# Kernel tuning notes

Hardware: AMD Instinct MI355X
Metric: run time of the kernel (lower is better)

Reference implementation:

```python
import jax, jax.numpy as jnp
import numpy as np

OUT, IN = 4096, 4096
GROUP = 128
N_GROUPS = IN // GROUP  # 32, remainder_cols == 0
BITS_PRIMARY = 4
BITS_RESIDUAL = 2
EPS = 1e-12


def setup_inputs() -> dict:
    key = jax.random.key(0)
    ks = jax.random.split(key, 6)
    return {
        "x": jax.random.normal(ks[0], (4, 2048, IN), dtype=jnp.float32),
        "norms_primary": jax.random.uniform(ks[1], (OUT, N_GROUPS), dtype=jnp.float32),
        "norms_residual": jax.random.uniform(ks[2], (OUT, N_GROUPS), dtype=jnp.float32),
        "bias": jax.random.normal(ks[3], (OUT,), dtype=jnp.float32),
        "idx_primary": jax.random.randint(ks[4], (OUT, N_GROUPS, GROUP), 0, 2 ** BITS_PRIMARY, dtype=jnp.int32),
        "idx_residual": jax.random.randint(ks[5], (OUT, N_GROUPS, GROUP), 0, 2 ** BITS_RESIDUAL, dtype=jnp.int32),
    }


def _dequant(idx, norms, bits):
    # Codebook: symmetric uniform levels in [-1, 1]; TurboQuant stores a
    # unit-direction per group (codes) plus its L2 norm (fp32 scale).
    levels = jnp.linspace(-1.0, 1.0, 2 ** bits, dtype=norms.dtype)
    q = levels[idx]                                             # [O, G, gs]
    unit = q * jax.lax.rsqrt(jnp.sum(q * q, axis=-1, keepdims=True) + EPS)
    w = norms[..., None] * unit                                 # [O, G, gs]
    return w.reshape(w.shape[0], -1)                            # [O, IN]


def reference(x, norms_primary, norms_residual, bias, idx_primary, idx_residual):
    # primary reconstruction + residual correction, then dense matmul
    w = _dequant(idx_primary, norms_primary, BITS_PRIMARY) \
        + _dequant(idx_residual, norms_residual, BITS_RESIDUAL)  # [OUT, IN]
    w = w.astype(x.dtype)
    # F.linear: y = x @ W^T + b
    return jnp.einsum('bsi,oi->bso', x, w) + bias.astype(x.dtype)
```

## Files before the change

### kernel.cpp

```cpp
#include <hip/hip_runtime.h>
#include <hip/hip_bf16.h>
#include <stdint.h>

#define OUT_DIM 4096
#define IN_DIM  4096
#define GROUPSZ 128
#define NGROUPS 32
#define M_TOTAL 8192
#define EPS_Q   1e-12f

#define BM 256
#define BN 256
#define BK 64
#define NT (IN_DIM / BK)

typedef float f32x4   __attribute__((ext_vector_type(4)));
typedef float float4v __attribute__((ext_vector_type(4)));
typedef short bf16x8  __attribute__((ext_vector_type(8)));

static __device__ __forceinline__ short f2bf(float f) {
    union { float f; unsigned u; } v; v.f = f;
    unsigned r = v.u + 0x7fffu + ((v.u >> 16) & 1u);
    return (short)(r >> 16);
}

#define GLOAD16(gp, lp) __builtin_amdgcn_global_load_lds( \
    (const __attribute__((address_space(1))) void*)(gp),  \
    (__attribute__((address_space(3))) void*)(lp), 16, 0, 0)

__global__ __launch_bounds__(256) void dequant_kernel(
    const float* __restrict__ norms_p, const float* __restrict__ norms_r,
    const int* __restrict__ idx_p, const int* __restrict__ idx_r,
    short* __restrict__ W)
{
    const int gid  = (int)((blockIdx.x * 256u + threadIdx.x) >> 6);
    const int lane = threadIdx.x & 63;
    const size_t base = (size_t)gid * GROUPSZ;

    const int ip0 = idx_p[base + lane];
    const int ip1 = idx_p[base + lane + 64];
    const int ir0 = idx_r[base + lane];
    const int ir1 = idx_r[base + lane + 64];

    const float qp0 = -1.f + (2.f / 15.f) * (float)ip0;
    const float qp1 = -1.f + (2.f / 15.f) * (float)ip1;
    const float qr0 = -1.f + (2.f / 3.f)  * (float)ir0;
    const float qr1 = -1.f + (2.f / 3.f)  * (float)ir1;

    float ssp = qp0 * qp0 + qp1 * qp1;
    float ssr = qr0 * qr0 + qr1 * qr1;
    #pragma unroll
    for (int m = 32; m >= 1; m >>= 1) {
        ssp += __shfl_xor(ssp, m);
        ssr += __shfl_xor(ssr, m);
    }
    const float sp = norms_p[gid] / sqrtf(ssp + EPS_Q);
    const float sr = norms_r[gid] / sqrtf(ssr + EPS_Q);

    W[base + lane]      = f2bf(qp0 * sp + qr0 * sr);
    W[base + lane + 64] = f2bf(qp1 * sp + qr1 * sr);
}

__global__ __launch_bounds__(256) void cast_kernel(
    const float* __restrict__ x, short* __restrict__ xb)
{
    const size_t i = ((size_t)blockIdx.x * 256u + threadIdx.x) * 8u;
    float4v a = *(const float4v*)(x + i);
    float4v b = *(const float4v*)(x + i + 4);
    bf16x8 o;
    o[0] = f2bf(a[0]); o[1] = f2bf(a[1]); o[2] = f2bf(a[2]); o[3] = f2bf(a[3]);
    o[4] = f2bf(b[0]); o[5] = f2bf(b[1]); o[6] = f2bf(b[2]); o[7] = f2bf(b[3]);
    *(bf16x8*)(xb + i) = o;
}

template<int HA, int HB>
__device__ __forceinline__ void mfma_quad(f32x4 (&acc)[2][2][4][2],
                                          const bf16x8 (&af)[4][2],
                                          const bf16x8 (&bf)[2][2]) {
#pragma unroll
    for (int m = 0; m < 4; ++m)
#pragma unroll
        for (int n = 0; n < 2; ++n)
#pragma unroll
            for (int kh = 0; kh < 2; ++kh)
                acc[HA][HB][m][n] = __builtin_amdgcn_mfma_f32_16x16x32_bf16(
                    af[m][kh], bf[n][kh], acc[HA][HB][m][n], 0, 0, 0);
}

static __device__ __forceinline__ void rd8(const short* base, int ck0, int ck1,
                                           bf16x8 (&f)[4][2]) {
#pragma unroll
    for (int m = 0; m < 4; ++m) {
        f[m][0] = *(const bf16x8*)(base + m * 1024 + ck0);
        f[m][1] = *(const bf16x8*)(base + m * 1024 + ck1);
    }
}

static __device__ __forceinline__ void rd4(const short* base, int ck0, int ck1,
                                           bf16x8 (&f)[2][2]) {
#pragma unroll
    for (int n = 0; n < 2; ++n) {
        f[n][0] = *(const bf16x8*)(base + n * 1024 + ck0);
        f[n][1] = *(const bf16x8*)(base + n * 1024 + ck1);
    }
}

#define BARRIER()  asm volatile("s_barrier" ::: "memory")
#define SCHEDBAR() __builtin_amdgcn_sched_barrier(0)
#define LGKMC(N)   do { asm volatile("s_waitcnt lgkmcnt(" #N ")" ::: "memory"); \
                        SCHEDBAR(); } while (0)
#define WAITV(N)   asm volatile("s_waitcnt vmcnt(" #N ")" ::: "memory")

__global__ __launch_bounds__(512, 2) void gemm_kernel(
    const short* __restrict__ Ag,
    const short* __restrict__ Bg,
    const float* __restrict__ bias,
    float* __restrict__ C)
{
    __shared__ short lds[65536];

    const int tid  = threadIdx.x;
    const int lane = tid & 63;
    const int wid  = tid >> 6;
    const int wr   = wid >> 2;
    const int wc   = wid & 3;
    const int fr   = lane & 15;
    const int lq   = lane >> 4;

    const int nwg = gridDim.x;
    const int cpx = nwg >> 3;
    const int wg  = ((int)blockIdx.x & 7) * cpx + ((int)blockIdx.x >> 3);
    const int ntile = wg & 15;
    const int mtile = wg >> 4;
    const uint32_t brow = (uint32_t)mtile * BM;
    const uint32_t bcol = (uint32_t)ntile * BN;

    const uint32_t sr_ = (uint32_t)(tid >> 3);
    const uint32_t gc_ = (uint32_t)((tid & 7) ^ ((tid >> 3) & 7));
    const uint32_t aOffB = (brow + sr_) * IN_DIM + gc_ * 8;
    const uint32_t bOffB = (bcol + sr_) * IN_DIM + gc_ * 8;

    auto stage = [&](const short* M, uint32_t baseOff, uint32_t extra, short* dstRegion) {
        GLOAD16(M + baseOff + extra,            dstRegion + tid * 8);
        GLOAD16(M + baseOff + extra + 262144u,  dstRegion + tid * 8 + 4096);
    };

    const int c0  = (lq ^ (fr & 7));
    const int ck0 = c0 * 8;
    const int ck1 = (c0 ^ 4) * 8;
    const int aRd = (wr * 64 + fr) * 64;
    const int bRd = (wc * 32 + fr) * 64;

    f32x4  acc[2][2][4][2] = {};
    bf16x8 af[4][2], af2[4][2], bf0[2][2], bf1[2][2];

    stage(Ag, aOffB, 0u,            lds);
    stage(Bg, bOffB, 0u,            lds + 16384);
    stage(Ag, aOffB, 524288u,       lds + 8192);
    stage(Bg, bOffB, 524288u,       lds + 24576);
    stage(Ag, aOffB, 64u,           lds + 32768);
    stage(Bg, bOffB, 64u,           lds + 32768 + 16384);
    WAITV(8);
    BARRIER();

#define TILE_BODY(T, STG0, STG1, STG2, STG3, WAIT_MID, WAIT_END, BAR_END) do { \
    short* sb = lds + (((T) & 1) ? 32768 : 0);                                \
    short* ob = lds + (((T) & 1) ? 0 : 32768);                                \
                              \
    rd8(sb + aRd, ck0, ck1, af);                                              \
    rd4(sb + 16384 + bRd, ck0, ck1, bf0);                                     \
    if (STG0) stage(Ag, aOffB, 524288u + (uint32_t)((T) + 1) * 64u, ob + 8192); \
    LGKMC(0);                                                                 \
    __builtin_amdgcn_s_setprio(1); mfma_quad<0,0>(acc, af, bf0);              \
    __builtin_amdgcn_s_setprio(0);                                            \
    WAIT_MID;                                                                 \
    BARRIER();                                                                \
                             \
    rd4(sb + 24576 + bRd, ck0, ck1, bf1);                                     \
    SCHEDBAR();                                                               \
    rd8(sb + 8192 + aRd, ck0, ck1, af2);                                      \
    if (STG1) stage(Bg, bOffB, 524288u + (uint32_t)((T) + 1) * 64u, ob + 24576); \
    LGKMC(8);                     \
    __builtin_amdgcn_s_setprio(1); mfma_quad<0,1>(acc, af, bf1);              \
    __builtin_amdgcn_s_setprio(0);                                            \
    if (STG2) stage(Ag, aOffB, (uint32_t)((T) + 2) * 64u, sb);                \
    LGKMC(0);                    \
    __builtin_amdgcn_s_setprio(1); mfma_quad<1,0>(acc, af2, bf0);             \
    __builtin_amdgcn_s_setprio(0);                                            \
    if (STG3) stage(Bg, bOffB, (uint32_t)((T) + 2) * 64u, sb + 16384);        \
    __builtin_amdgcn_s_setprio(1); mfma_quad<1,1>(acc, af2, bf1);             \
    __builtin_amdgcn_s_setprio(0);                                            \
    WAIT_END;                                                                 \
    if (BAR_END) BARRIER();                                                   \
} while (0)

    #pragma unroll 1
    for (int t = 0; t < NT - 2; ++t) {
        TILE_BODY(t, 1, 1, 1, 1, WAITV(6), WAITV(8), 1);
    }
    TILE_BODY(NT - 2, 1, 1, 0, 0, WAITV(6), WAITV(4), 1);
    TILE_BODY(NT - 1, 0, 0, 0, 0, WAITV(0), (void)0, 0);

    #pragma unroll
    for (int hA = 0; hA < 2; ++hA)
    #pragma unroll
    for (int hB = 0; hB < 2; ++hB)
    #pragma unroll
    for (int n = 0; n < 2; ++n) {
        const int col = (int)bcol + hB * 128 + wc * 32 + n * 16 + fr;
        const float bv = bias[col];
        #pragma unroll
        for (int m = 0; m < 4; ++m) {
            const size_t row0 = (size_t)brow + hA * 128 + wr * 64 + m * 16 + lq * 4;
            #pragma unroll
            for (int r = 0; r < 4; ++r)
                C[(row0 + r) * OUT_DIM + col] = acc[hA][hB][m][n][r] + bv;
        }
    }
#undef TILE_BODY
}

extern "C" void kernel_launch(void* const* d_in, const int* in_sizes, int n_in,
                              void* d_out, int out_size, void* d_ws, size_t ws_size,
                              hipStream_t stream)
{
    const float* x        = (const float*)d_in[0];
    const float* norms_p  = (const float*)d_in[1];
    const float* norms_r  = (const float*)d_in[2];
    const float* bias     = (const float*)d_in[3];
    const int*   idx_p    = (const int*)d_in[4];
    const int*   idx_r    = (const int*)d_in[5];
    float*       out      = (float*)d_out;

    short* xb = (short*)d_ws;
    short* wq = (short*)d_ws + (size_t)M_TOTAL * IN_DIM;

    dequant_kernel<<<(OUT_DIM * NGROUPS) / 4, 256, 0, stream>>>(
        norms_p, norms_r, idx_p, idx_r, wq);

    cast_kernel<<<(int)(((size_t)M_TOTAL * IN_DIM) / (256 * 8)), 256, 0, stream>>>(x, xb);

    gemm_kernel<<<(M_TOTAL / BM) * (OUT_DIM / BN), 512, 0, stream>>>(xb, wq, bias, out);
}
```

Measured before the change: 281.2 us.

## Restructure GEMM main loop into barrier-synchronized phases with reordered quadrant staging

Rewrites the bf16 MFMA GEMM main loop as a two-tile unrolled group body. LDS reads, global-to-LDS stage issues and the four MFMA quadrants now sit in separate phases divided by workgroup barriers, and the quadrant order and per-quadrant staging order change. The prologue now prefetches one more quarter-tile so the steady state can keep more loads in flight. The aim is more regular overlap of loads with compute across waves, at the cost of many more barriers per tile, which could serialize waves.

```diff
diff --git a/kernel.cpp b/kernel.cpp
--- a/kernel.cpp
+++ b/kernel.cpp
@@ -154,52 +154,61 @@
     f32x4  acc[2][2][4][2] = {};
     bf16x8 af[4][2], af2[4][2], bf0[2][2], bf1[2][2];
 
-    stage(Ag, aOffB, 0u,            lds);
-    stage(Bg, bOffB, 0u,            lds + 16384);
-    stage(Ag, aOffB, 524288u,       lds + 8192);
-    stage(Bg, bOffB, 524288u,       lds + 24576);
-    stage(Ag, aOffB, 64u,           lds + 32768);
-    stage(Bg, bOffB, 64u,           lds + 32768 + 16384);
-    WAITV(8);
+    stage(Ag, aOffB, 0u,             lds);
+    stage(Bg, bOffB, 0u,             lds + 16384);
+    stage(Bg, bOffB, 524288u,        lds + 24576);
+    stage(Ag, aOffB, 524288u,        lds + 8192);
+    stage(Ag, aOffB, 64u,            lds + 32768);
+    stage(Bg, bOffB, 64u,            lds + 32768 + 16384);
+    stage(Bg, bOffB, 524288u + 64u,  lds + 32768 + 24576);
+    WAITV(6);
     BARRIER();
 
-#define TILE_BODY(T, STG0, STG1, STG2, STG3, WAIT_MID, WAIT_END, BAR_END) do { \
-    short* sb = lds + (((T) & 1) ? 32768 : 0);                                \
-    short* ob = lds + (((T) & 1) ? 0 : 32768);                                \
-                              \
-    rd8(sb + aRd, ck0, ck1, af);                                              \
-    rd4(sb + 16384 + bRd, ck0, ck1, bf0);                                     \
-    if (STG0) stage(Ag, aOffB, 524288u + (uint32_t)((T) + 1) * 64u, ob + 8192); \
+#define GROUP_BODY(SB, OB, TT, S_A1, S_A0, S_B0, S_B1, WAIT_END) do {         \
+                  \
+    rd8((SB) + aRd, ck0, ck1, af);                                            \
+    rd4((SB) + 16384 + bRd, ck0, ck1, bf0);                                   \
+    if (S_A1) stage(Ag, aOffB, 524288u + (uint32_t)((TT)+1)*64u, (OB)+8192);  \
+    LGKMC(8);                                                                 \
+    BARRIER();                                                                \
     LGKMC(0);                                                                 \
     __builtin_amdgcn_s_setprio(1); mfma_quad<0,0>(acc, af, bf0);              \
     __builtin_amdgcn_s_setprio(0);                                            \
-    WAIT_MID;                                                                 \
-    BARRIER();                                                                \
-                             \
-    rd4(sb + 24576 + bRd, ck0, ck1, bf1);                                     \
+    BARRIER();                                                                \
+                         \
+    rd4((SB) + 24576 + bRd, ck0, ck1, bf1);                                   \
+    if (S_A0) stage(Ag, aOffB, (uint32_t)((TT)+2)*64u, (SB));                 \
+    BARRIER();                                                                \
+    LGKMC(0);                                                                 \
+    __builtin_amdgcn_s_setprio(1); mfma_quad<0,1>(acc, af, bf1);              \
+    __builtin_amdgcn_s_setprio(0);                                            \
+    BARRIER();                                                                \
+                         \
+    rd8((SB) + 8192 + aRd, ck0, ck1, af2);                                    \
+    if (S_B0) stage(Bg, bOffB, (uint32_t)((TT)+2)*64u, (SB)+16384);           \
+    BARRIER();                                                                \
+    LGKMC(0);                                                                 \
+    __builtin_amdgcn_s_setprio(1); mfma_quad<1,1>(acc, af2, bf1);             \
+    __builtin_amdgcn_s_setprio(0);                                            \
+    BARRIER();                                                                \
+                    \
+    if (S_B1) stage(Bg, bOffB, 524288u + (uint32_t)((TT)+2)*64u, (SB)+24576); \
+    BARRIER();                                                                \
     SCHEDBAR();                                                               \
-    rd8(sb + 8192 + aRd, ck0, ck1, af2);                                      \
-    if (STG1) stage(Bg, bOffB, 524288u + (uint32_t)((T) + 1) * 64u, ob + 24576); \
-    LGKMC(8);                     \
-    __builtin_amdgcn_s_setprio(1); mfma_quad<0,1>(acc, af, bf1);              \
-    __builtin_amdgcn_s_setprio(0);                                            \
-    if (STG2) stage(Ag, aOffB, (uint32_t)((T) + 2) * 64u, sb);                \
-    LGKMC(0);                    \
     __builtin_amdgcn_s_setprio(1); mfma_quad<1,0>(acc, af2, bf0);             \
     __builtin_amdgcn_s_setprio(0);                                            \
-    if (STG3) stage(Bg, bOffB, (uint32_t)((T) + 2) * 64u, sb + 16384);        \
-    __builtin_amdgcn_s_setprio(1); mfma_quad<1,1>(acc, af2, bf1);             \
-    __builtin_amdgcn_s_setprio(0);                                            \
     WAIT_END;                                                                 \
-    if (BAR_END) BARRIER();                                                   \
+    BARRIER();                                                                \
 } while (0)
 
     #pragma unroll 1
-    for (int t = 0; t < NT - 2; ++t) {
-        TILE_BODY(t, 1, 1, 1, 1, WAITV(6), WAITV(8), 1);
-    }
-    TILE_BODY(NT - 2, 1, 1, 0, 0, WAITV(6), WAITV(4), 1);
-    TILE_BODY(NT - 1, 0, 0, 0, 0, WAITV(0), (void)0, 0);
+    for (int t = 0; t < NT - 2; t += 2) {
+        GROUP_BODY(lds,         lds + 32768, t,     1, 1, 1, 1, WAITV(6));
+        GROUP_BODY(lds + 32768, lds,         t + 1, 1, 1, 1, 1, WAITV(6));
+    }
+    GROUP_BODY(lds,         lds + 32768, NT - 2, 1, 0, 0, 0, WAITV(0));
+    GROUP_BODY(lds + 32768, lds,         NT - 1, 0, 0, 0, 0, (void)0);
+#undef GROUP_BODY
 
     #pragma unroll
     for (int hA = 0; hA < 2; ++hA)
@@ -217,7 +226,6 @@
                 C[(row0 + r) * OUT_DIM + col] = acc[hA][hB][m][n][r] + bv;
         }
     }
-#undef TILE_BODY
 }
 
 extern "C" void kernel_launch(void* const* d_in, const int* in_sizes, int n_in,
```

Result: no change. 284.3 us (+1.1%).

## Load B fragments directly to registers and deepen A LDS pipeline to four stages

Applied to the files above, without the earlier changes.

The GEMM no longer stages the weight (B) tile through LDS. Each wave now gathers its B fragments straight from global memory into double-buffered registers one tile ahead. A tiles use a four-slot LDS ring filled three tiles ahead, and the last MFMA quad of each tile is deferred into the next tile to overlap with LDS reads. This is meant to cut LDS traffic and barriers per K-step, at the cost of more register pressure and uncoalesced, non-shared B global loads, since waves in the same column fetch the same data.

```diff
diff --git a/kernel.cpp b/kernel.cpp
--- a/kernel.cpp
+++ b/kernel.cpp
@@ -96,20 +96,13 @@
     }
 }
 
-static __device__ __forceinline__ void rd4(const short* base, int ck0, int ck1,
-                                           bf16x8 (&f)[2][2]) {
-#pragma unroll
-    for (int n = 0; n < 2; ++n) {
-        f[n][0] = *(const bf16x8*)(base + n * 1024 + ck0);
-        f[n][1] = *(const bf16x8*)(base + n * 1024 + ck1);
-    }
-}
-
 #define BARRIER()  asm volatile("s_barrier" ::: "memory")
 #define SCHEDBAR() __builtin_amdgcn_sched_barrier(0)
 #define LGKMC(N)   do { asm volatile("s_waitcnt lgkmcnt(" #N ")" ::: "memory"); \
                         SCHEDBAR(); } while (0)
 #define WAITV(N)   asm volatile("s_waitcnt vmcnt(" #N ")" ::: "memory")
+#define PRIO1()    __builtin_amdgcn_s_setprio(1)
+#define PRIO0()    __builtin_amdgcn_s_setprio(0)
 
 __global__ __launch_bounds__(512, 2) void gemm_kernel(
     const short* __restrict__ Ag,
@@ -137,69 +130,76 @@
 
     const uint32_t sr_ = (uint32_t)(tid >> 3);
     const uint32_t gc_ = (uint32_t)((tid & 7) ^ ((tid >> 3) & 7));
-    const uint32_t aOffB = (brow + sr_) * IN_DIM + gc_ * 8;
-    const uint32_t bOffB = (bcol + sr_) * IN_DIM + gc_ * 8;
-
-    auto stage = [&](const short* M, uint32_t baseOff, uint32_t extra, short* dstRegion) {
-        GLOAD16(M + baseOff + extra,            dstRegion + tid * 8);
-        GLOAD16(M + baseOff + extra + 262144u,  dstRegion + tid * 8 + 4096);
+    const size_t aOff = (size_t)(brow + sr_) * IN_DIM + gc_ * 8;
+
+    auto stageA = [&](int t) {
+        short* dst = lds + (t & 3) * 16384;
+        const short* src = Ag + aOff + (size_t)t * 64;
+        #pragma unroll
+        for (int k = 0; k < 4; ++k)
+            GLOAD16(src + k * 262144, dst + (tid + k * 512) * 8);
+    };
+
+    const short* bBase = Bg + (size_t)(bcol + wc * 32 + fr) * IN_DIM + lq * 8;
+    auto gatherB = [&](int t, bf16x8 (&b)[2][2][2]) {
+        const short* p = bBase + (size_t)t * 64;
+        #pragma unroll
+        for (int hB = 0; hB < 2; ++hB)
+        #pragma unroll
+        for (int n = 0; n < 2; ++n)
+        #pragma unroll
+        for (int kh = 0; kh < 2; ++kh)
+            b[hB][n][kh] = *(const bf16x8*)(p + hB * 524288 + n * 65536 + kh * 32);
     };
 
     const int c0  = (lq ^ (fr & 7));
     const int ck0 = c0 * 8;
     const int ck1 = (c0 ^ 4) * 8;
     const int aRd = (wr * 64 + fr) * 64;
-    const int bRd = (wc * 32 + fr) * 64;
 
     f32x4  acc[2][2][4][2] = {};
-    bf16x8 af[4][2], af2[4][2], bf0[2][2], bf1[2][2];
-
-    stage(Ag, aOffB, 0u,            lds);
-    stage(Bg, bOffB, 0u,            lds + 16384);
-    stage(Ag, aOffB, 524288u,       lds + 8192);
-    stage(Bg, bOffB, 524288u,       lds + 24576);
-    stage(Ag, aOffB, 64u,           lds + 32768);
-    stage(Bg, bOffB, 64u,           lds + 32768 + 16384);
-    WAITV(8);
+    bf16x8 af[4][2], af2[4][2];
+    bf16x8 bA[2][2][2], bB[2][2][2];
+
+    stageA(0);
+    stageA(1);
+    gatherB(0, bB);
+    stageA(2);
+    SCHEDBAR();
+    WAITV(16);
     BARRIER();
 
-#define TILE_BODY(T, STG0, STG1, STG2, STG3, WAIT_MID, WAIT_END, BAR_END) do { \
-    short* sb = lds + (((T) & 1) ? 32768 : 0);                                \
-    short* ob = lds + (((T) & 1) ? 0 : 32768);                                \
-                              \
+#define TILE(T, BCUR, BPREV, PEND, GATH, STG, WAIT_N, DO_TAIL) do {           \
+    short* sb = lds + ((T) & 3) * 16384;                                      \
     rd8(sb + aRd, ck0, ck1, af);                                              \
-    rd4(sb + 16384 + bRd, ck0, ck1, bf0);                                     \
-    if (STG0) stage(Ag, aOffB, 524288u + (uint32_t)((T) + 1) * 64u, ob + 8192); \
+    SCHEDBAR();                                                               \
+    if (PEND) { PRIO1(); mfma_quad<1,1>(acc, af2, BPREV[1]); PRIO0(); }       \
+    SCHEDBAR();                                                               \
+    rd8(sb + aRd + 8192, ck0, ck1, af2);                                      \
+    if (GATH) gatherB((T) + 1, BPREV);                                        \
+    if (STG)  stageA((T) + 3);                                                \
+    SCHEDBAR();                                                               \
+    WAIT_N;                                                                   \
     LGKMC(0);                                                                 \
-    __builtin_amdgcn_s_setprio(1); mfma_quad<0,0>(acc, af, bf0);              \
-    __builtin_amdgcn_s_setprio(0);                                            \
-    WAIT_MID;                                                                 \
+    PRIO1();                                                                  \
+    mfma_quad<0,0>(acc, af, BCUR[0]);                                         \
+    mfma_quad<0,1>(acc, af, BCUR[1]);                                         \
+    mfma_quad<1,0>(acc, af2, BCUR[0]);                                        \
+    if (DO_TAIL) mfma_quad<1,1>(acc, af2, BCUR[1]);                           \
+    PRIO0();                                                                  \
     BARRIER();                                                                \
-                             \
-    rd4(sb + 24576 + bRd, ck0, ck1, bf1);                                     \
-    SCHEDBAR();                                                               \
-    rd8(sb + 8192 + aRd, ck0, ck1, af2);                                      \
-    if (STG1) stage(Bg, bOffB, 524288u + (uint32_t)((T) + 1) * 64u, ob + 24576); \
-    LGKMC(8);                     \
-    __builtin_amdgcn_s_setprio(1); mfma_quad<0,1>(acc, af, bf1);              \
-    __builtin_amdgcn_s_setprio(0);                                            \
-    if (STG2) stage(Ag, aOffB, (uint32_t)((T) + 2) * 64u, sb);                \
-    LGKMC(0);                    \
-    __builtin_amdgcn_s_setprio(1); mfma_quad<1,0>(acc, af2, bf0);             \
-    __builtin_amdgcn_s_setprio(0);                                            \
-    if (STG3) stage(Bg, bOffB, (uint32_t)((T) + 2) * 64u, sb + 16384);        \
-    __builtin_amdgcn_s_setprio(1); mfma_quad<1,1>(acc, af2, bf1);             \
-    __builtin_amdgcn_s_setprio(0);                                            \
-    WAIT_END;                                                                 \
-    if (BAR_END) BARRIER();                                                   \
 } while (0)
 
+    TILE(0, bB, bA, 0, 1, 1, WAITV(16), 0);
     #pragma unroll 1
-    for (int t = 0; t < NT - 2; ++t) {
-        TILE_BODY(t, 1, 1, 1, 1, WAITV(6), WAITV(8), 1);
-    }
-    TILE_BODY(NT - 2, 1, 1, 0, 0, WAITV(6), WAITV(4), 1);
-    TILE_BODY(NT - 1, 0, 0, 0, 0, WAITV(0), (void)0, 0);
+    for (int t = 1; t < NT - 4; t += 2) {
+        TILE(t,     bA, bB, 1, 1, 1, WAITV(16), 0);
+        TILE(t + 1, bB, bA, 1, 1, 1, WAITV(16), 0);
+    }
+    TILE(NT - 3, bA, bB, 1, 1, 0, WAITV(12), 0);
+    TILE(NT - 2, bB, bA, 1, 1, 0, WAITV(8),  0);
+    TILE(NT - 1, bA, bB, 1, 0, 0, WAITV(0),  1);
+#undef TILE
 
     #pragma unroll
     for (int hA = 0; hA < 2; ++hA)
@@ -217,7 +217,6 @@
                 C[(row0 + r) * OUT_DIM + col] = acc[hA][hB][m][n][r] + bv;
         }
     }
-#undef TILE_BODY
 }
 
 extern "C" void kernel_launch(void* const* d_in, const int* in_sizes, int n_in,
```

After: 857.8 us. +205.0%, slower.
